# Kernel tuning notes

Hardware: AMD Instinct MI355X
Metric: run time of the kernel (lower is better)

## Reference

```python
import jax, jax.numpy as jnp
import numpy as np

BITS = 4
MAXQ = (1 << BITS) - 1  # 15
GROUPSIZE = 128
IN_F = 8192
OUT_F = 8192
PACK = 32 // BITS  # 8 values per int32


def setup_inputs() -> dict:
    key = jax.random.key(0)
    k_x, k_w, k_z, k_s, k_b = jax.random.split(key, 5)
    groups = IN_F // GROUPSIZE
    x = jax.random.normal(k_x, (4, 32, IN_F), dtype=jnp.float32)
    # bit-packed int32 weight / zeros (random bit patterns are valid quantized data)
    qweight = jax.random.randint(k_w, (IN_F // PACK, OUT_F), 0, 2**31 - 1, dtype=jnp.int32)
    qzeros = jax.random.randint(k_z, (groups, OUT_F // PACK), 0, 2**31 - 1, dtype=jnp.int32)
    scales = (jax.random.uniform(k_s, (groups, OUT_F), dtype=jnp.float32) * 0.01 + 1e-3)
    g_idx = (jnp.arange(IN_F, dtype=jnp.int32) // GROUPSIZE).astype(jnp.int32)
    bias = jax.random.normal(k_b, (OUT_F,), dtype=jnp.float32) * 0.01
    return {"x": x, "qweight": qweight, "qzeros": qzeros, "scales": scales,
            "g_idx": g_idx, "bias": bias}


def _dequant(qweight, qzeros, scales, g_idx):
    shifts = jnp.arange(0, 32, BITS, dtype=jnp.int32)  # [PACK]
    # unpack weights along the input dim: [in/PACK, PACK, out] -> [in, out]
    w = (qweight[:, None, :] >> shifts[None, :, None]) & MAXQ
    w = w.reshape(-1, qweight.shape[1])
    # unpack zeros along the output dim: [groups, out/PACK, PACK] -> [groups, out]
    # GPTQ stores (zero - 1), so add 1 back
    z = ((qzeros[:, :, None] >> shifts[None, None, :]) & MAXQ) + 1
    z = z.reshape(qzeros.shape[0], -1)
    # per-group dequant: W[i, o] = scales[g_idx[i], o] * (w[i, o] - z[g_idx[i], o])
    W = scales[g_idx] * (w.astype(scales.dtype) - z[g_idx].astype(scales.dtype))
    return W  # [in, out]


def reference(x, qweight, qzeros, scales, g_idx, bias):
    W = _dequant(qweight, qzeros, scales, g_idx)
    out = jnp.einsum('bsi,io->bso', x, W) + bias
    return out
```

## Files before the change

kernel.cpp:

```cpp
#include <hip/hip_runtime.h>
#include <hip/hip_bf16.h>
#include <stdint.h>


#define IN_F 8192
#define OUT_F 8192

typedef short short8_t __attribute__((ext_vector_type(8)));
typedef float float4_t __attribute__((ext_vector_type(4)));
typedef float float16_t __attribute__((ext_vector_type(16)));

__global__ __launch_bounds__(1024, 4) void gptq_fused(
    const float* __restrict__ x,
    const int* __restrict__ qweight,
    const int* __restrict__ qzeros,
    const float* __restrict__ scales,
    const float* __restrict__ bias,
    float* __restrict__ out)
{
  __shared__ __align__(16) unsigned short As[2][64 * 512];

  const int tid  = threadIdx.x;
  const int lane = tid & 63;
  const int l31  = lane & 31;
  const int half = lane >> 5;
  const int wv   = tid >> 6;
  const int ph   = wv & 3;
  const int wc   = (wv >> 2) & 1;
  const int wr   = wv >> 3;

  const int bid = blockIdx.x;
  const int mb  = bid >> 7;
  const int nb  = bid & 127;
  const int m0  = mb * 64;
  const int col = nb * 64 + wc * 32 + l31;

  const int kp_base = ph * 16 + half;

  int   qw[2][8];
  float sc[2];
  int   zq[2];

  auto qpref = [&](int c, int buf) {
    const int kp0 = c * 64 + kp_base;
#pragma unroll
    for (int ks = 0; ks < 8; ++ks)
      qw[buf][ks] = qweight[(size_t)(kp0 + ks * 2) * OUT_F + col];
    const int gg = c * 4 + ph;
    sc[buf] = scales[gg * OUT_F + col];
    zq[buf] = qzeros[gg * (OUT_F / 8) + (col >> 3)];
  };

  float4_t sa[4], sb[4];
  auto stage_load = [&](int c) {
#pragma unroll
    for (int rq = 0; rq < 4; ++rq) {
      const int rl = wv * 4 + rq;
      const float* grow = x + (size_t)(m0 + rl) * IN_F + c * 512;
      const int cc = (lane & ~15) | ((lane ^ (rl & 15)) & 15);
      sa[rq] = *(const float4_t*)(grow + cc * 8);
      sb[rq] = *(const float4_t*)(grow + cc * 8 + 4);
    }
  };
  auto stage_write = [&](int b) {
#pragma unroll
    for (int rq = 0; rq < 4; ++rq) {
      const int rl = wv * 4 + rq;
      union { short8_t v; __hip_bfloat162 h[4]; } u;
      u.h[0] = __float22bfloat162_rn(make_float2(sa[rq].x, sa[rq].y));
      u.h[1] = __float22bfloat162_rn(make_float2(sa[rq].z, sa[rq].w));
      u.h[2] = __float22bfloat162_rn(make_float2(sb[rq].x, sb[rq].y));
      u.h[3] = __float22bfloat162_rn(make_float2(sb[rq].z, sb[rq].w));
      *(short8_t*)(&As[b][((size_t)rl * 64 + lane) * 8]) = u.v;
    }
  };

  qpref(0, 0);
  stage_load(0);
  stage_write(0);
  __syncthreads();

  float16_t acc;
#pragma unroll
  for (int r = 0; r < 16; ++r) acc[r] = 0.f;

#pragma unroll 2
  for (int c = 0; c < 16; ++c) {
    const int cur = c & 1;

    if (c + 1 < 16) { qpref(c + 1, cur ^ 1); stage_load(c + 1); }

    const int z = ((zq[cur] >> (4 * (col & 7))) & 15) + 1;
    const float zb = -sc[cur] * (float)z;
    const float s = sc[cur];

#pragma unroll
    for (int ks = 0; ks < 8; ++ks) {
      const int cL = ph * 16 + ks * 2 + half;
      const int p  = (cL & ~15) | ((cL ^ (l31 & 15)) & 15);
      const short8_t af =
          *(const short8_t*)(&As[cur][((size_t)(wr * 32 + l31) * 64 + p) * 8]);

      union { short8_t v; unsigned u[4]; } bw;
      const unsigned q  = (unsigned)qw[cur][ks];
      const unsigned qe = q & 0x0F0F0F0Fu;
      const unsigned qo = (q >> 4) & 0x0F0F0F0Fu;
#pragma unroll
      for (int jj = 0; jj < 4; ++jj) {
        const float f0 = fmaf(s, (float)((qe >> (8 * jj)) & 0xffu), zb);
        const float f1 = fmaf(s, (float)((qo >> (8 * jj)) & 0xffu), zb);
        bw.u[jj] = __builtin_amdgcn_perm(__float_as_uint(f1), __float_as_uint(f0),
                                         0x07060302u);
      }

      acc = __builtin_amdgcn_mfma_f32_32x32x16_bf16(af, bw.v, acc, 0, 0, 0);
    }

    if (c + 1 < 16) stage_write(cur ^ 1);
    __syncthreads();
  }

  float* Ms = (float*)&As[0][0];
  const int tile = wr * 2 + wc;
  if (ph != 0) {
    float* dst = Ms + (size_t)((tile * 3 + (ph - 1)) * 64 + lane) * 20;
#pragma unroll
    for (int q4 = 0; q4 < 4; ++q4) {
      float4_t v;
      v.x = acc[q4 * 4 + 0]; v.y = acc[q4 * 4 + 1];
      v.z = acc[q4 * 4 + 2]; v.w = acc[q4 * 4 + 3];
      *(float4_t*)(dst + q4 * 4) = v;
    }
  }
  __syncthreads();
  if (ph == 0) {
#pragma unroll
    for (int j = 0; j < 3; ++j) {
      const float* src = Ms + (size_t)((tile * 3 + j) * 64 + lane) * 20;
#pragma unroll
      for (int q4 = 0; q4 < 4; ++q4) {
        float4_t v = *(const float4_t*)(src + q4 * 4);
        acc[q4 * 4 + 0] += v.x; acc[q4 * 4 + 1] += v.y;
        acc[q4 * 4 + 2] += v.z; acc[q4 * 4 + 3] += v.w;
      }
    }
    const float bcol = bias[col];
#pragma unroll
    for (int r = 0; r < 16; ++r) {
      const int row = (r & 3) + 8 * (r >> 2) + 4 * half;
      out[(size_t)(m0 + wr * 32 + row) * OUT_F + col] = acc[r] + bcol;
    }
  }
}

extern "C" void kernel_launch(void* const* d_in, const int* in_sizes, int n_in,
                              void* d_out, int out_size, void* d_ws, size_t ws_size,
                              hipStream_t stream) {
  const float* x        = (const float*)d_in[0];
  const int*   qweight  = (const int*)d_in[1];
  const int*   qzeros   = (const int*)d_in[2];
  const float* scales   = (const float*)d_in[3];
  const float* bias     = (const float*)d_in[5];
  float* out = (float*)d_out;

  (void)d_ws; (void)ws_size;

  gptq_fused<<<dim3(256), 1024, 0, stream>>>(x, qweight, qzeros, scales, bias, out);
}
```

Measured before the change: 123.2 us.

## Halve M tile per block and deepen split-K to eight waves

Each block now covers 32 rows instead of 64, doubling the grid to 512 blocks, and the 16 waves split as 2 column tiles by 8 K-slices instead of 2 by 2 by 4. This aims to raise CU occupancy and parallelism for a grid that previously gave only one block per CU. The cost is that each quantized weight tile is loaded and dequantized by two blocks instead of one, and the cross-wave LDS reduction grows to seven partials.

```diff
diff --git a/kernel.cpp b/kernel.cpp
--- a/kernel.cpp
+++ b/kernel.cpp
@@ -10,7 +10,7 @@
 typedef float float4_t __attribute__((ext_vector_type(4)));
 typedef float float16_t __attribute__((ext_vector_type(16)));
 
-__global__ __launch_bounds__(1024, 4) void gptq_fused(
+__global__ __launch_bounds__(1024, 8) void gptq_fused2(
     const float* __restrict__ x,
     const int* __restrict__ qweight,
     const int* __restrict__ qzeros,
@@ -18,61 +18,65 @@
     const float* __restrict__ bias,
     float* __restrict__ out)
 {
-  __shared__ __align__(16) unsigned short As[2][64 * 512];
+  __shared__ __align__(16) unsigned short As[2][32 * 512 + 1600];
 
   const int tid  = threadIdx.x;
   const int lane = tid & 63;
   const int l31  = lane & 31;
   const int half = lane >> 5;
   const int wv   = tid >> 6;
-  const int ph   = wv & 3;
-  const int wc   = (wv >> 2) & 1;
-  const int wr   = wv >> 3;
+  const int ph   = wv & 7;
+  const int wc   = wv >> 3;
+  const int gl   = ph >> 1;
+  const int hl   = ph & 1;
 
   const int bid = blockIdx.x;
   const int mb  = bid >> 7;
   const int nb  = bid & 127;
-  const int m0  = mb * 64;
+  const int m0  = mb * 32;
   const int col = nb * 64 + wc * 32 + l31;
 
-  const int kp_base = ph * 16 + half;
+  const int kp_base = gl * 16 + hl * 8 + half;
 
-  int   qw[2][8];
+  int   qw[2][4];
   float sc[2];
   int   zq[2];
 
   auto qpref = [&](int c, int buf) {
     const int kp0 = c * 64 + kp_base;
 #pragma unroll
-    for (int ks = 0; ks < 8; ++ks)
+    for (int ks = 0; ks < 4; ++ks)
       qw[buf][ks] = qweight[(size_t)(kp0 + ks * 2) * OUT_F + col];
-    const int gg = c * 4 + ph;
+    const int gg = c * 4 + gl;
     sc[buf] = scales[gg * OUT_F + col];
     zq[buf] = qzeros[gg * (OUT_F / 8) + (col >> 3)];
   };
 
-  float4_t sa[4], sb[4];
+  const int u0r = tid >> 6;
+  const int u0p = tid & 63;
+  float4_t sa0, sb0, sa1, sb1;
   auto stage_load = [&](int c) {
-#pragma unroll
-    for (int rq = 0; rq < 4; ++rq) {
-      const int rl = wv * 4 + rq;
-      const float* grow = x + (size_t)(m0 + rl) * IN_F + c * 512;
-      const int cc = (lane & ~15) | ((lane ^ (rl & 15)) & 15);
-      sa[rq] = *(const float4_t*)(grow + cc * 8);
-      sb[rq] = *(const float4_t*)(grow + cc * 8 + 4);
-    }
+    const int cc0 = (u0p & ~15) | ((u0p ^ (u0r & 15)) & 15);
+    const int cc1 = (u0p & ~15) | ((u0p ^ ((u0r + 16) & 15)) & 15);
+    const float* g0 = x + (size_t)(m0 + u0r) * IN_F + c * 512 + cc0 * 8;
+    const float* g1 = x + (size_t)(m0 + u0r + 16) * IN_F + c * 512 + cc1 * 8;
+    sa0 = *(const float4_t*)(g0);
+    sb0 = *(const float4_t*)(g0 + 4);
+    sa1 = *(const float4_t*)(g1);
+    sb1 = *(const float4_t*)(g1 + 4);
   };
   auto stage_write = [&](int b) {
-#pragma unroll
-    for (int rq = 0; rq < 4; ++rq) {
-      const int rl = wv * 4 + rq;
-      union { short8_t v; __hip_bfloat162 h[4]; } u;
-      u.h[0] = __float22bfloat162_rn(make_float2(sa[rq].x, sa[rq].y));
-      u.h[1] = __float22bfloat162_rn(make_float2(sa[rq].z, sa[rq].w));
-      u.h[2] = __float22bfloat162_rn(make_float2(sb[rq].x, sb[rq].y));
-      u.h[3] = __float22bfloat162_rn(make_float2(sb[rq].z, sb[rq].w));
-      *(short8_t*)(&As[b][((size_t)rl * 64 + lane) * 8]) = u.v;
-    }
+    union { short8_t v; __hip_bfloat162 h[4]; } u;
+    u.h[0] = __float22bfloat162_rn(make_float2(sa0.x, sa0.y));
+    u.h[1] = __float22bfloat162_rn(make_float2(sa0.z, sa0.w));
+    u.h[2] = __float22bfloat162_rn(make_float2(sb0.x, sb0.y));
+    u.h[3] = __float22bfloat162_rn(make_float2(sb0.z, sb0.w));
+    *(short8_t*)(&As[b][((size_t)u0r * 64 + u0p) * 8]) = u.v;
+    u.h[0] = __float22bfloat162_rn(make_float2(sa1.x, sa1.y));
+    u.h[1] = __float22bfloat162_rn(make_float2(sa1.z, sa1.w));
+    u.h[2] = __float22bfloat162_rn(make_float2(sb1.x, sb1.y));
+    u.h[3] = __float22bfloat162_rn(make_float2(sb1.z, sb1.w));
+    *(short8_t*)(&As[b][((size_t)(u0r + 16) * 64 + u0p) * 8]) = u.v;
   };
 
   qpref(0, 0);
@@ -95,11 +99,11 @@
     const float s = sc[cur];
 
 #pragma unroll
-    for (int ks = 0; ks < 8; ++ks) {
-      const int cL = ph * 16 + ks * 2 + half;
+    for (int ks = 0; ks < 4; ++ks) {
+      const int cL = gl * 16 + hl * 8 + ks * 2 + half;
       const int p  = (cL & ~15) | ((cL ^ (l31 & 15)) & 15);
       const short8_t af =
-          *(const short8_t*)(&As[cur][((size_t)(wr * 32 + l31) * 64 + p) * 8]);
+          *(const short8_t*)(&As[cur][((size_t)l31 * 64 + p) * 8]);
 
       union { short8_t v; unsigned u[4]; } bw;
       const unsigned q  = (unsigned)qw[cur][ks];
@@ -121,9 +125,8 @@
   }
 
   float* Ms = (float*)&As[0][0];
-  const int tile = wr * 2 + wc;
   if (ph != 0) {
-    float* dst = Ms + (size_t)((tile * 3 + (ph - 1)) * 64 + lane) * 20;
+    float* dst = Ms + (size_t)((wc * 7 + (ph - 1)) * 64 + lane) * 20;
 #pragma unroll
     for (int q4 = 0; q4 < 4; ++q4) {
       float4_t v;
@@ -135,8 +138,8 @@
   __syncthreads();
   if (ph == 0) {
 #pragma unroll
-    for (int j = 0; j < 3; ++j) {
-      const float* src = Ms + (size_t)((tile * 3 + j) * 64 + lane) * 20;
+    for (int j = 0; j < 7; ++j) {
+      const float* src = Ms + (size_t)((wc * 7 + j) * 64 + lane) * 20;
 #pragma unroll
       for (int q4 = 0; q4 < 4; ++q4) {
         float4_t v = *(const float4_t*)(src + q4 * 4);
@@ -148,7 +151,7 @@
 #pragma unroll
     for (int r = 0; r < 16; ++r) {
       const int row = (r & 3) + 8 * (r >> 2) + 4 * half;
-      out[(size_t)(m0 + wr * 32 + row) * OUT_F + col] = acc[r] + bcol;
+      out[(size_t)(m0 + row) * OUT_F + col] = acc[r] + bcol;
     }
   }
 }
@@ -165,5 +168,5 @@
 
   (void)d_ws; (void)ws_size;
 
-  gptq_fused<<<dim3(256), 1024, 0, stream>>>(x, qweight, qzeros, scales, bias, out);
+  gptq_fused2<<<dim3(512), 1024, 0, stream>>>(x, qweight, qzeros, scales, bias, out);
 }
```

Measured after the change: 222.7 us. +80.8%, slower.
